# Optimization experiments

Measured on AMD Instinct MI355X. Metric: run time of the kernel, lower is better.

The kernel has to match this reference:

```python
import jax, jax.numpy as jnp
import numpy as np

ROPE_DIMS = 64  # rope_rotary_dims == head_dim, so RoPE covers full head


def fixed_pos_embedding(max_len, rotary_dims):
    inv_freq = 1.0 / (10000 ** (jnp.arange(0, rotary_dims, 2, dtype=jnp.float32) / rotary_dims))
    sinusoid = jnp.einsum('i,j->ij', jnp.arange(max_len, dtype=jnp.float32), inv_freq)
    return jnp.sin(sinusoid), jnp.cos(sinusoid)


def rotate_every_two(x):
    x1 = x[..., ::2]
    x2 = x[..., 1::2]
    return jnp.stack((-x2, x1), axis=-1).reshape(x.shape)


def apply_rotary_pos_emb(x, sin, cos):
    # x: [B, L, H, D]; sin/cos: [L, D//2]
    L = x.shape[1]
    sin = jnp.repeat(sin[:L], 2, axis=-1)[None, :, None, :]  # interleaved repeat == .repeat(2, axis=3)
    cos = jnp.repeat(cos[:L], 2, axis=-1)[None, :, None, :]
    return x * cos + rotate_every_two(x) * sin


def setup_inputs() -> dict:
    key = jax.random.key(0)
    ks = jax.random.split(key, 8)
    B, Lq, Lkv, F, H, D = 2, 2048, 2048, 1024, 16, 64
    s = 0.02
    return {
        'inputs_q': jax.random.normal(ks[0], (B, Lq, F), dtype=jnp.float32),
        'inputs_kv': jax.random.normal(ks[1], (B, Lkv, F), dtype=jnp.float32),
        'mask': jax.random.randint(ks[2], (B, 1, Lq, Lkv), 0, 2) > 0,
        'Wq': jax.random.normal(ks[3], (F, H, D), dtype=jnp.float32) * s,
        'bq': jnp.zeros((H, D), dtype=jnp.float32),
        'Wk': jax.random.normal(ks[4], (F, D), dtype=jnp.float32) * s,
        'bk': jnp.zeros((D,), dtype=jnp.float32),
        'Wv': jax.random.normal(ks[5], (F, D), dtype=jnp.float32) * s,
        'bv': jnp.zeros((D,), dtype=jnp.float32),
        'Wo': jax.random.normal(ks[6], (H, D, F), dtype=jnp.float32) * s,
        'bo': jnp.zeros((F,), dtype=jnp.float32),
    }


def reference(inputs_q, inputs_kv, mask, Wq, bq, Wk, bk, Wv, bv, Wo, bo):
    D = Wq.shape[-1]
    Lq, Lkv = inputs_q.shape[1], inputs_kv.shape[1]
    # QKV projections (multi-query: single shared K/V head)
    q = jnp.einsum('blf,fhd->blhd', inputs_q, Wq) + bq   # [B,Lq,H,D]
    k = jnp.einsum('blf,fd->bld', inputs_kv, Wk) + bk    # [B,Lkv,D]
    v = jnp.einsum('blf,fd->bld', inputs_kv, Wv) + bv    # [B,Lkv,D]
    # RoPE on q and (head-expanded) k
    sin, cos = fixed_pos_embedding(max(Lq, Lkv), ROPE_DIMS)
    q = apply_rotary_pos_emb(q, sin, cos)
    k = apply_rotary_pos_emb(k[:, :, None, :], sin, cos)[:, :, 0, :]
    # multi-query attention
    q = q / jnp.sqrt(jnp.float32(D))
    attn = jnp.einsum('bqhd,bkd->bhqk', q, k)            # [B,H,Lq,Lkv]
    big_neg = jnp.finfo(jnp.float32).min
    attn = jnp.where(mask, attn, big_neg)
    attn = jax.nn.softmax(attn, axis=-1)
    out = jnp.einsum('bhqk,bkd->bqhd', attn, v)          # [B,Lq,H,D]
    # output projection
    return jnp.einsum('bqhd,hdf->bqf', out, Wo) + bo     # [B,Lq,F]
```

## Files before the change

### kernel.cpp

```cpp
#include <hip/hip_runtime.h>

typedef unsigned short u16;
typedef unsigned int u32;
typedef unsigned long long u64;
typedef __bf16 bf16x8 __attribute__((ext_vector_type(8)));
typedef u16 u16x8 __attribute__((ext_vector_type(8)));
typedef float f32x4 __attribute__((ext_vector_type(4)));

__device__ __forceinline__ u16 f2bf(float f) {
    return __builtin_bit_cast(u16, (__bf16)f);
}

__device__ __forceinline__ void gl_lds16(const void* g, void* l) {
    __builtin_amdgcn_global_load_lds(
        (const __attribute__((address_space(1))) unsigned int*)g,
        (__attribute__((address_space(3))) unsigned int*)l, 16, 0, 0);
}

#define QSCALE 0.18033688011112042f

__global__ void detect_mask(const unsigned char* __restrict__ m, int* __restrict__ flag,
                            float* __restrict__ lut) {
    int t = threadIdx.x;
    lut[t] = (((t >> 2) >> (t & 3)) & 1) ? -16.0f : -100000.0f;
    if (t == 0) {
        int any0 = 0, any1 = 0;
        for (int g = 0; g < 64; ++g) {
            any0 |= (m[4 * g] != 0);
            any1 |= (m[4 * g + 1] != 0);
        }
        *flag = any1 ? 0 : (any0 ? 1 : 2);
    }
}

__global__ void prep(const float4* __restrict__ inq, const float4* __restrict__ inkv,
                     ushort4* __restrict__ oAq, ushort4* __restrict__ oAkv,
                     const float* __restrict__ Wq, const float* __restrict__ Wk,
                     const float* __restrict__ Wv, const float* __restrict__ Wo,
                     u16* __restrict__ Wcat, u16* __restrict__ Wot,
                     const void* __restrict__ mask, const int* __restrict__ flagp,
                     u64* __restrict__ Mb, float2* __restrict__ rtbl) {
    int bid = blockIdx.x;
    const int tid = threadIdx.x;
    if (bid < 8192) {
        int i = bid * 256 + tid;
        const float4* src; ushort4* dst; int j;
        if (i < 1048576) { src = inq;  dst = oAq;  j = i; }
        else             { src = inkv; dst = oAkv; j = i - 1048576; }
        float4 f = src[j];
        ushort4 o;
        o.x = f2bf(f.x); o.y = f2bf(f.y); o.z = f2bf(f.z); o.w = f2bf(f.w);
        dst[j] = o;
        return;
    }
    bid -= 8192;
    if (bid < 2176) {
        const float* src; u16* dst; int C, bx, by;
        if (bid < 1024)      { src = Wq; dst = Wcat;           C = 1024; bx = bid & 31;          by = bid >> 5; }
        else if (bid < 2048) { src = Wo; dst = Wot;            C = 1024; bx = (bid - 1024) & 31; by = (bid - 1024) >> 5; }
        else if (bid < 2112) { src = Wk; dst = Wcat + 1048576; C = 64;   bx = (bid - 2048) & 1;  by = (bid - 2048) >> 1; }
        else                 { src = Wv; dst = Wcat + 1114112; C = 64;   bx = (bid - 2112) & 1;  by = (bid - 2112) >> 1; }
        __shared__ float t[32][33];
        int tx = tid & 31, ty = tid >> 5;
        bx *= 32; by *= 32;
#pragma unroll
        for (int i = 0; i < 4; ++i)
            t[ty + i * 8][tx] = src[(size_t)(by + ty + i * 8) * C + bx + tx];
        __syncthreads();
#pragma unroll
        for (int i = 0; i < 4; ++i)
            dst[(size_t)(bx + ty + i * 8) * 1024 + by + tx] = f2bf(t[tx][ty + i * 8]);
        return;
    }
    bid -= 2176;
    if (bid < 256) {
        int i = bid * 256 + tid;
        int pos = i >> 5, j = i & 31;
        float inv = powf(10000.0f, -(float)(2 * j) * (1.0f / 64.0f));
        float s, c;
        sincosf((float)pos * inv, &s, &c);
        rtbl[i] = make_float2(c, s);
        return;
    }
    bid -= 256;
    {
        int flag = *flagp;
        int lane = tid & 63;
        for (int wid = bid * 4 + (tid >> 6); wid < 131072; wid += 8192) {
            size_t idx = (size_t)wid * 64 + lane;
            bool v;
            if (flag == 0)      v = ((const unsigned char*)mask)[idx] != 0;
            else if (flag == 1) v = ((const int*)mask)[idx] != 0;
            else                v = ((const float*)mask)[idx] != 0.f;
            u64 bm = __ballot(v);
            if (lane == 0) Mb[wid] = bm;
        }
    }
}

template <int MODE>
__launch_bounds__(256)
__global__ void gemm_bt(const u16* __restrict__ A0, const u16* __restrict__ A1,
                        const u16* __restrict__ Bt,
                        const float* __restrict__ b1, const float* __restrict__ b2,
                        const float* __restrict__ b3,
                        const float2* __restrict__ rtbl,
                        u16* __restrict__ oQ, u16* __restrict__ oK, u16* __restrict__ oV,
                        float* __restrict__ oF, int Ntiles) {
    __shared__ __align__(16) u16 lA[2][64 * 64];
    __shared__ __align__(16) u16 lB[2][128 * 64];
    const int tid = threadIdx.x, w = tid >> 6, lane = tid & 63;
    const int tm = blockIdx.x / Ntiles, tn = blockIdx.x % Ntiles;
    const int wm = w >> 1, wn = w & 1;
    const int lq = lane & 15, g = lane >> 4, g4 = g << 2;
    const u32 swz = (lane & 7) << 4;
    const u32 bcolg = (16 * g) ^ swz;
    const u16* A = (MODE == 0 && tn == 8) ? A1 : A0;

    const int rA0 = tid >> 3, ch = tid & 7;
    const int rB0 = rA0;
    const u32 offc = ((u32)(ch << 4)) ^ ((u32)((rA0 & 7) << 4));
    const u16* pA0 = A + (size_t)(tm * 64 + rA0) * 1024 + ch * 8;
    const u16* pA1 = pA0 + 32 * 1024;
    const u16* pB0 = Bt + (size_t)(tn * 128 + rB0) * 1024 + ch * 8;
    const u16* pB1 = pB0 + 32 * 1024;
    const u16* pB2 = pB0 + 64 * 1024;
    const u16* pB3 = pB0 + 96 * 1024;
    const u32 offA0 = rA0 * 128 + offc, offA1 = offA0 + 32 * 128;
    const u32 offB0 = offA0, offB1 = offB0 + 32 * 128, offB2 = offB0 + 64 * 128,
              offB3 = offB0 + 96 * 128;

    u16x8 ra0, ra1, rb0, rb1, rb2, rb3;
    f32x4 acc[2][4] = {};

    ra0 = *(const u16x8*)(pA0); ra1 = *(const u16x8*)(pA1);
    rb0 = *(const u16x8*)(pB0); rb1 = *(const u16x8*)(pB1);
    rb2 = *(const u16x8*)(pB2); rb3 = *(const u16x8*)(pB3);
    *(u16x8*)((char*)lA + offA0) = ra0; *(u16x8*)((char*)lA + offA1) = ra1;
    *(u16x8*)((char*)lB + offB0) = rb0; *(u16x8*)((char*)lB + offB1) = rb1;
    *(u16x8*)((char*)lB + offB2) = rb2; *(u16x8*)((char*)lB + offB3) = rb3;
    __syncthreads();

#pragma unroll
    for (int t = 0; t < 16; ++t) {
        if (t < 15) {
            ra0 = *(const u16x8*)(pA0 + (t + 1) * 64); ra1 = *(const u16x8*)(pA1 + (t + 1) * 64);
            rb0 = *(const u16x8*)(pB0 + (t + 1) * 64); rb1 = *(const u16x8*)(pB1 + (t + 1) * 64);
            rb2 = *(const u16x8*)(pB2 + (t + 1) * 64); rb3 = *(const u16x8*)(pB3 + (t + 1) * 64);
        }
        const char* bA = (const char*)lA + (t & 1) * 8192;
        const char* bB = (const char*)lB + (t & 1) * 16384;
#pragma unroll
        for (int kc = 0; kc < 2; ++kc) {
            const u32 col = bcolg ^ (64 * kc);
            bf16x8 af0 = *(const bf16x8*)(bA + (wm * 32 + lq) * 128 + col);
            bf16x8 af1 = *(const bf16x8*)(bA + (wm * 32 + 16 + lq) * 128 + col);
            bf16x8 bg0 = *(const bf16x8*)(bB + (wn * 64 + lq) * 128 + col);
            bf16x8 bg1 = *(const bf16x8*)(bB + (wn * 64 + 16 + lq) * 128 + col);
            bf16x8 bg2 = *(const bf16x8*)(bB + (wn * 64 + 32 + lq) * 128 + col);
            bf16x8 bg3 = *(const bf16x8*)(bB + (wn * 64 + 48 + lq) * 128 + col);
            acc[0][0] = __builtin_amdgcn_mfma_f32_16x16x32_bf16(af0, bg0, acc[0][0], 0, 0, 0);
            acc[0][1] = __builtin_amdgcn_mfma_f32_16x16x32_bf16(af0, bg1, acc[0][1], 0, 0, 0);
            acc[0][2] = __builtin_amdgcn_mfma_f32_16x16x32_bf16(af0, bg2, acc[0][2], 0, 0, 0);
            acc[0][3] = __builtin_amdgcn_mfma_f32_16x16x32_bf16(af0, bg3, acc[0][3], 0, 0, 0);
            acc[1][0] = __builtin_amdgcn_mfma_f32_16x16x32_bf16(af1, bg0, acc[1][0], 0, 0, 0);
            acc[1][1] = __builtin_amdgcn_mfma_f32_16x16x32_bf16(af1, bg1, acc[1][1], 0, 0, 0);
            acc[1][2] = __builtin_amdgcn_mfma_f32_16x16x32_bf16(af1, bg2, acc[1][2], 0, 0, 0);
            acc[1][3] = __builtin_amdgcn_mfma_f32_16x16x32_bf16(af1, bg3, acc[1][3], 0, 0, 0);
        }
        if (t < 15) {
            char* nA = (char*)lA + ((t + 1) & 1) * 8192;
            char* nB = (char*)lB + ((t + 1) & 1) * 16384;
            *(u16x8*)(nA + offA0) = ra0; *(u16x8*)(nA + offA1) = ra1;
            *(u16x8*)(nB + offB0) = rb0; *(u16x8*)(nB + offB1) = rb1;
            *(u16x8*)(nB + offB2) = rb2; *(u16x8*)(nB + offB3) = rb3;
        }
        __syncthreads();
    }

#pragma unroll
    for (int mi = 0; mi < 2; ++mi) {
#pragma unroll
        for (int ni = 0; ni < 4; ++ni) {
#pragma unroll
            for (int r = 0; r < 4; ++r) {
                int grow = tm * 64 + wm * 32 + mi * 16 + g4 + r;
                float v = acc[mi][ni][r];
                if constexpr (MODE == 0) {
                    int pos = grow & 2047;
                    if (tn < 8) {
                        int gcol = tn * 128 + wn * 64 + ni * 16 + lq;
                        v += b1[gcol];
                        float2 cs = rtbl[pos * 32 + ((gcol & 63) >> 1)];
                        float prt = __shfl_xor(v, 1);
                        v = (gcol & 1) ? (v * cs.x + prt * cs.y) : (v * cs.x - prt * cs.y);
                        v *= QSCALE;
                        oQ[(size_t)grow * 1024 + gcol] = f2bf(v);
                    } else {
                        int lc = wn * 64 + ni * 16 + lq;
                        if (lc < 64) {
                            v += b2[lc];
                            float2 cs = rtbl[pos * 32 + (lc >> 1)];
                            float prt = __shfl_xor(v, 1);
                            v = (lc & 1) ? (v * cs.x + prt * cs.y) : (v * cs.x - prt * cs.y);
                            oK[(size_t)grow * 64 + lc] = f2bf(v);
                        } else {
                            int d = lc - 64;
                            v += b3[d];
                            int b = grow >> 11, ll = grow & 2047;
                            oV[((size_t)(b * 64 + d)) * 2048 + ll] = f2bf(v);
                        }
                    }
                } else {
                    int gcol = tn * 128 + wn * 64 + ni * 16 + lq;
                    oF[(size_t)grow * 1024 + gcol] = v + b1[gcol];
                }
            }
        }
    }
}

__launch_bounds__(256, 4)
__global__ void flash(const u16* __restrict__ Qb, const u16* __restrict__ Kb,
                      const u16* __restrict__ Vt, const u64* __restrict__ Mb,
                      const f32x4* __restrict__ lut, u16* __restrict__ Ob) {
    __shared__ __align__(16) u16 lK[2][64 * 64];
    __shared__ __align__(16) u16 lV[2][64 * 64];
    __shared__ __align__(16) u16 lP[4 * 16 * 64];
    const int tid = threadIdx.x, w = tid >> 6, lane = tid & 63;
    const int qt = blockIdx.x & 31, h = (blockIdx.x >> 5) & 15, b = blockIdx.x >> 9;
    const int qb = qt * 64 + w * 16;
    const int lq = lane & 15, g = lane >> 4, g4 = g << 2;
    const u32 swz = (lq & 7) << 4;
    const u32 rowoff = lq * 128;
    const u32 bcol = ((u32)(16 * g)) ^ swz;
    const u32 bw = ((u32)(8 * g)) ^ swz;
    char* lPw = (char*)lP + w * 2048;
    const int sh = 4 * g;

    bf16x8 qf0, qf1;
    {
        const u16* qp = Qb + (size_t)(b * 2048 + qb + lq) * 1024 + h * 64 + g * 8;
        qf0 = *(const bf16x8*)(qp);
        qf1 = *(const bf16x8*)(qp + 32);
    }

    const u64* Mrow = Mb + (size_t)(b * 2048 + qb + lq) * 32;

    const int rs = tid >> 3, ch = tid & 7;
    const u32 scb = (((u32)(ch << 4)) ^ ((u32)((rs & 7) << 4))) >> 1;
    const u16* pK0 = Kb + (size_t)(b * 2048 + rs) * 64 + scb;
    const u16* pK1 = pK0 + 32 * 64;
    const u16* pV0 = Vt + (size_t)(b * 64 + rs) * 2048 + scb;
    const u16* pV1 = pV0 + 32 * 2048;
    char* dK = (char*)lK + tid * 16;
    char* dV = (char*)lV + tid * 16;

#define STAGE(BUF)                                                   \
    {                                                                \
        gl_lds16(pK0, dK + (BUF) * 8192);                            \
        gl_lds16(pK1, dK + (BUF) * 8192 + 4096);                     \
        gl_lds16(pV0, dV + (BUF) * 8192);                            \
        gl_lds16(pV1, dV + (BUF) * 8192 + 4096);                     \
        pK0 += 4096; pK1 += 4096; pV0 += 64; pV1 += 64;              \
    }

    f32x4 o0 = {}, o1 = {}, o2 = {}, o3 = {};
    float lsum = 0.f;

    f32x4 iA0, iA1, iA2, iA3, iB0, iB1, iB2, iB3;
    u64 mwA, mwB;
    {
        u64 ms = Mrow[0] >> sh;
        u32 lo = (u32)ms, hi = (u32)(ms >> 32);
        iA0 = lut[lo & 15]; iA1 = lut[(lo >> 16) & 15];
        iA2 = lut[hi & 15]; iA3 = lut[(hi >> 16) & 15];
    }
    mwA = Mrow[1];
    STAGE(0);
    __syncthreads();

#define EXPPK(NF, S)                                                                    \
    {                                                                                   \
        float p0 = exp2f(S[0]), p1 = exp2f(S[1]), p2 = exp2f(S[2]), p3 = exp2f(S[3]);   \
        lsum += (p0 + p1) + (p2 + p3);                                                  \
        uint2 pk_;                                                                      \
        pk_.x = (u32)f2bf(p0) | ((u32)f2bf(p1) << 16);                                  \
        pk_.y = (u32)f2bf(p2) | ((u32)f2bf(p3) << 16);                                  \
        *(uint2*)(lPw + rowoff + (bw ^ (32 * NF))) = pk_;                               \
    }

#define COMPUTE(BUF, I0, I1, I2, I3, N0, N1, N2, N3, MWC, MWN, KC)                      \
    {                                                                                   \
        MWN = Mrow[(KC) + 2];                                                           \
        {                                                                               \
            u64 ms = MWC >> sh;                                                         \
            u32 lo = (u32)ms, hi = (u32)(ms >> 32);                                     \
            N0 = lut[lo & 15]; N1 = lut[(lo >> 16) & 15];                               \
            N2 = lut[hi & 15]; N3 = lut[(hi >> 16) & 15];                               \
        }                                                                               \
        f32x4 s0 = I0, s1 = I1, s2 = I2, s3 = I3;                                       \
        {                                                                               \
            const char* kb_ = (const char*)lK + (BUF) * 8192 + rowoff;                  \
            bf16x8 k00 = *(const bf16x8*)(kb_ + bcol);                                  \
            bf16x8 k01 = *(const bf16x8*)(kb_ + (bcol ^ 64));                           \
            bf16x8 k10 = *(const bf16x8*)(kb_ + 2048 + bcol);                           \
            bf16x8 k11 = *(const bf16x8*)(kb_ + 2048 + (bcol ^ 64));                    \
            bf16x8 k20 = *(const bf16x8*)(kb_ + 4096 + bcol);                           \
            bf16x8 k21 = *(const bf16x8*)(kb_ + 4096 + (bcol ^ 64));                    \
            bf16x8 k30 = *(const bf16x8*)(kb_ + 6144 + bcol);                           \
            bf16x8 k31 = *(const bf16x8*)(kb_ + 6144 + (bcol ^ 64));                    \
            s0 = __builtin_amdgcn_mfma_f32_16x16x32_bf16(k00, qf0, s0, 0, 0, 0);        \
            s0 = __builtin_amdgcn_mfma_f32_16x16x32_bf16(k01, qf1, s0, 0, 0, 0);        \
            s1 = __builtin_amdgcn_mfma_f32_16x16x32_bf16(k10, qf0, s1, 0, 0, 0);        \
            s1 = __builtin_amdgcn_mfma_f32_16x16x32_bf16(k11, qf1, s1, 0, 0, 0);        \
            s2 = __builtin_amdgcn_mfma_f32_16x16x32_bf16(k20, qf0, s2, 0, 0, 0);        \
            s2 = __builtin_amdgcn_mfma_f32_16x16x32_bf16(k21, qf1, s2, 0, 0, 0);        \
            s3 = __builtin_amdgcn_mfma_f32_16x16x32_bf16(k30, qf0, s3, 0, 0, 0);        \
            s3 = __builtin_amdgcn_mfma_f32_16x16x32_bf16(k31, qf1, s3, 0, 0, 0);        \
        }                                                                               \
        EXPPK(0, s0) EXPPK(1, s1) EXPPK(2, s2) EXPPK(3, s3)                             \
        {                                                                               \
            bf16x8 pf0 = *(const bf16x8*)(lPw + rowoff + bcol);                         \
            bf16x8 pf1 = *(const bf16x8*)(lPw + rowoff + (bcol ^ 64));                  \
            const char* vb_ = (const char*)lV + (BUF) * 8192 + rowoff;                  \
            bf16x8 v00 = *(const bf16x8*)(vb_ + bcol);                                  \
            bf16x8 v01 = *(const bf16x8*)(vb_ + (bcol ^ 64));                           \
            bf16x8 v10 = *(const bf16x8*)(vb_ + 2048 + bcol);                           \
            bf16x8 v11 = *(const bf16x8*)(vb_ + 2048 + (bcol ^ 64));                    \
            bf16x8 v20 = *(const bf16x8*)(vb_ + 4096 + bcol);                           \
            bf16x8 v21 = *(const bf16x8*)(vb_ + 4096 + (bcol ^ 64));                    \
            bf16x8 v30 = *(const bf16x8*)(vb_ + 6144 + bcol);                           \
            bf16x8 v31 = *(const bf16x8*)(vb_ + 6144 + (bcol ^ 64));                    \
            o0 = __builtin_amdgcn_mfma_f32_16x16x32_bf16(pf0, v00, o0, 0, 0, 0);        \
            o0 = __builtin_amdgcn_mfma_f32_16x16x32_bf16(pf1, v01, o0, 0, 0, 0);        \
            o1 = __builtin_amdgcn_mfma_f32_16x16x32_bf16(pf0, v10, o1, 0, 0, 0);        \
            o1 = __builtin_amdgcn_mfma_f32_16x16x32_bf16(pf1, v11, o1, 0, 0, 0);        \
            o2 = __builtin_amdgcn_mfma_f32_16x16x32_bf16(pf0, v20, o2, 0, 0, 0);        \
            o2 = __builtin_amdgcn_mfma_f32_16x16x32_bf16(pf1, v21, o2, 0, 0, 0);        \
            o3 = __builtin_amdgcn_mfma_f32_16x16x32_bf16(pf0, v30, o3, 0, 0, 0);        \
            o3 = __builtin_amdgcn_mfma_f32_16x16x32_bf16(pf1, v31, o3, 0, 0, 0);        \
        }                                                                               \
    }

    for (int kc = 0; kc < 32; kc += 2) {
        STAGE(1);
        COMPUTE(0, iA0, iA1, iA2, iA3, iB0, iB1, iB2, iB3, mwA, mwB, kc);
        __syncthreads();
        STAGE(0);
        COMPUTE(1, iB0, iB1, iB2, iB3, iA0, iA1, iA2, iA3, mwB, mwA, kc + 1);
        __syncthreads();
    }
#undef STAGE
#undef COMPUTE
#undef EXPPK

    lsum += __shfl_xor(lsum, 16);
    lsum += __shfl_xor(lsum, 32);
    float rl0 = 1.0f / __shfl(lsum, g4);
    float rl1 = 1.0f / __shfl(lsum, g4 + 1);
    float rl2 = 1.0f / __shfl(lsum, g4 + 2);
    float rl3 = 1.0f / __shfl(lsum, g4 + 3);
    {
        int col = h * 64 + lq;
        size_t base = (size_t)(b * 2048 + qb + g4) * 1024 + col;
        Ob[base]              = f2bf(o0[0] * rl0);
        Ob[base + 1024]       = f2bf(o0[1] * rl1);
        Ob[base + 2048]       = f2bf(o0[2] * rl2);
        Ob[base + 3072]       = f2bf(o0[3] * rl3);
        Ob[base + 16]         = f2bf(o1[0] * rl0);
        Ob[base + 16 + 1024]  = f2bf(o1[1] * rl1);
        Ob[base + 16 + 2048]  = f2bf(o1[2] * rl2);
        Ob[base + 16 + 3072]  = f2bf(o1[3] * rl3);
        Ob[base + 32]         = f2bf(o2[0] * rl0);
        Ob[base + 32 + 1024]  = f2bf(o2[1] * rl1);
        Ob[base + 32 + 2048]  = f2bf(o2[2] * rl2);
        Ob[base + 32 + 3072]  = f2bf(o2[3] * rl3);
        Ob[base + 48]         = f2bf(o3[0] * rl0);
        Ob[base + 48 + 1024]  = f2bf(o3[1] * rl1);
        Ob[base + 48 + 2048]  = f2bf(o3[2] * rl2);
        Ob[base + 48 + 3072]  = f2bf(o3[3] * rl3);
    }
}

extern "C" void kernel_launch(void* const* d_in, const int* in_sizes, int n_in,
                              void* d_out, int out_size, void* d_ws, size_t ws_size,
                              hipStream_t stream) {
    (void)in_sizes; (void)n_in; (void)out_size; (void)ws_size;
    const float* inq  = (const float*)d_in[0];
    const float* inkv = (const float*)d_in[1];
    const void*  mask = d_in[2];
    const float* Wq   = (const float*)d_in[3];
    const float* bq   = (const float*)d_in[4];
    const float* Wk   = (const float*)d_in[5];
    const float* bk   = (const float*)d_in[6];
    const float* Wv   = (const float*)d_in[7];
    const float* bv   = (const float*)d_in[8];
    const float* Wo   = (const float*)d_in[9];
    const float* bo   = (const float*)d_in[10];
    float* out = (float*)d_out;

    char* ws = (char*)d_ws;
    int* flag    = (int*)ws;
    f32x4* lut   = (f32x4*)(ws + 256);
    u16* Aq   = (u16*)(ws + 512);
    u16* Akv  = Aq + 4194304;
    u16* Wcat = Akv + 4194304;
    u16* Wot  = Wcat + 1179648;
    u16* Qb   = Wot + 1048576;
    u16* Kbf  = Qb + 4194304;
    u16* Vtb  = Kbf + 266496;
    u16* Ob   = Vtb + 266496;
    u64* Mb   = (u64*)(Ob + 4194304);
    float2* rtbl = (float2*)(Mb + 131080);

    detect_mask<<<1, 64, 0, stream>>>((const unsigned char*)mask, flag, (float*)lut);
    prep<<<12672, 256, 0, stream>>>((const float4*)inq, (const float4*)inkv,
                                    (ushort4*)Aq, (ushort4*)Akv,
                                    Wq, Wk, Wv, Wo, Wcat, Wot,
                                    mask, flag, Mb, rtbl);
    gemm_bt<0><<<576, 256, 0, stream>>>(Aq, Akv, Wcat, bq, bk, bv, rtbl,
                                        Qb, Kbf, Vtb, nullptr, 9);
    flash<<<1024, 256, 0, stream>>>(Qb, Kbf, Vtb, Mb, lut, Ob);
    gemm_bt<2><<<512, 256, 0, stream>>>(Ob, nullptr, Wot, bo, nullptr, nullptr, rtbl,
                                        nullptr, nullptr, nullptr, out, 8);
}
```

Before: 139.1 us.

## Rewrite flash attention with 32x32 MFMA, register-resident P, swizzled K/V layout

Result: slower. 153.2 us (+10.1%).

```diff
diff --git a/kernel.cpp b/kernel.cpp
--- a/kernel.cpp
+++ b/kernel.cpp
@@ -4,8 +4,11 @@
 typedef unsigned int u32;
 typedef unsigned long long u64;
 typedef __bf16 bf16x8 __attribute__((ext_vector_type(8)));
+typedef __bf16 bf16x4 __attribute__((ext_vector_type(4)));
 typedef u16 u16x8 __attribute__((ext_vector_type(8)));
 typedef float f32x4 __attribute__((ext_vector_type(4)));
+typedef float f32x16 __attribute__((ext_vector_type(16)));
+typedef u32 u32x4 __attribute__((ext_vector_type(4)));
 
 __device__ __forceinline__ u16 f2bf(float f) {
     return __builtin_bit_cast(u16, (__bf16)f);
@@ -118,11 +121,10 @@
     const u16* A = (MODE == 0 && tn == 8) ? A1 : A0;
 
     const int rA0 = tid >> 3, ch = tid & 7;
-    const int rB0 = rA0;
     const u32 offc = ((u32)(ch << 4)) ^ ((u32)((rA0 & 7) << 4));
     const u16* pA0 = A + (size_t)(tm * 64 + rA0) * 1024 + ch * 8;
     const u16* pA1 = pA0 + 32 * 1024;
-    const u16* pB0 = Bt + (size_t)(tn * 128 + rB0) * 1024 + ch * 8;
+    const u16* pB0 = Bt + (size_t)(tn * 128 + rA0) * 1024 + ch * 8;
     const u16* pB1 = pB0 + 32 * 1024;
     const u16* pB2 = pB0 + 64 * 1024;
     const u16* pB3 = pB0 + 96 * 1024;
@@ -203,12 +205,15 @@
                             float2 cs = rtbl[pos * 32 + (lc >> 1)];
                             float prt = __shfl_xor(v, 1);
                             v = (lc & 1) ? (v * cs.x + prt * cs.y) : (v * cs.x - prt * cs.y);
-                            oK[(size_t)grow * 64 + lc] = f2bf(v);
+                            oK[(size_t)grow * 64 + ((((u32)lc >> 2) ^ ((u32)grow & 15)) << 2)
+                               + (lc & 3)] = f2bf(v);
                         } else {
                             int d = lc - 64;
                             v += b3[d];
                             int b = grow >> 11, ll = grow & 2047;
-                            oV[((size_t)(b * 64 + d)) * 2048 + ll] = f2bf(v);
+                            int cc = ll & 63;
+                            oV[((size_t)(b * 64 + d)) * 2048 + (ll & ~63)
+                               + ((((u32)cc >> 2) ^ ((u32)d & 15)) << 2) + (cc & 3)] = f2bf(v);
                         }
                     }
                 } else {
@@ -220,166 +225,163 @@
     }
 }
 
-__launch_bounds__(256, 4)
+#define MFMA32(A, B, C) __builtin_amdgcn_mfma_f32_32x32x16_bf16(A, B, C, 0, 0, 0)
+
+__launch_bounds__(256)
 __global__ void flash(const u16* __restrict__ Qb, const u16* __restrict__ Kb,
                       const u16* __restrict__ Vt, const u64* __restrict__ Mb,
                       const f32x4* __restrict__ lut, u16* __restrict__ Ob) {
     __shared__ __align__(16) u16 lK[2][64 * 64];
     __shared__ __align__(16) u16 lV[2][64 * 64];
-    __shared__ __align__(16) u16 lP[4 * 16 * 64];
     const int tid = threadIdx.x, w = tid >> 6, lane = tid & 63;
-    const int qt = blockIdx.x & 31, h = (blockIdx.x >> 5) & 15, b = blockIdx.x >> 9;
-    const int qb = qt * 64 + w * 16;
-    const int lq = lane & 15, g = lane >> 4, g4 = g << 2;
-    const u32 swz = (lq & 7) << 4;
-    const u32 rowoff = lq * 128;
-    const u32 bcol = ((u32)(16 * g)) ^ swz;
-    const u32 bw = ((u32)(8 * g)) ^ swz;
-    char* lPw = (char*)lP + w * 2048;
-    const int sh = 4 * g;
-
-    bf16x8 qf0, qf1;
+    const int qt = blockIdx.x & 15, hh = (blockIdx.x >> 4) & 15, b = blockIdx.x >> 8;
+    const int qb = qt * 128 + w * 32;
+    const int l31 = lane & 31, h = lane >> 5, l15 = lane & 15;
+
+    bf16x8 qf0, qf1, qf2, qf3;
     {
-        const u16* qp = Qb + (size_t)(b * 2048 + qb + lq) * 1024 + h * 64 + g * 8;
+        const u16* qp = Qb + (size_t)(b * 2048 + qb + l31) * 1024 + hh * 64 + h * 8;
         qf0 = *(const bf16x8*)(qp);
-        qf1 = *(const bf16x8*)(qp + 32);
-    }
-
-    const u64* Mrow = Mb + (size_t)(b * 2048 + qb + lq) * 32;
-
-    const int rs = tid >> 3, ch = tid & 7;
-    const u32 scb = (((u32)(ch << 4)) ^ ((u32)((rs & 7) << 4))) >> 1;
-    const u16* pK0 = Kb + (size_t)(b * 2048 + rs) * 64 + scb;
-    const u16* pK1 = pK0 + 32 * 64;
-    const u16* pV0 = Vt + (size_t)(b * 64 + rs) * 2048 + scb;
-    const u16* pV1 = pV0 + 32 * 2048;
-    char* dK = (char*)lK + tid * 16;
-    char* dV = (char*)lV + tid * 16;
-
-#define STAGE(BUF)                                                   \
-    {                                                                \
-        gl_lds16(pK0, dK + (BUF) * 8192);                            \
-        gl_lds16(pK1, dK + (BUF) * 8192 + 4096);                     \
-        gl_lds16(pV0, dV + (BUF) * 8192);                            \
-        gl_lds16(pV1, dV + (BUF) * 8192 + 4096);                     \
-        pK0 += 4096; pK1 += 4096; pV0 += 64; pV1 += 64;              \
-    }
-
-    f32x4 o0 = {}, o1 = {}, o2 = {}, o3 = {};
+        qf1 = *(const bf16x8*)(qp + 16);
+        qf2 = *(const bf16x8*)(qp + 32);
+        qf3 = *(const bf16x8*)(qp + 48);
+    }
+
+    const u64* Mrow = Mb + (size_t)(b * 2048 + qb + l31) * 32;
+
+    u32 dof0 = ((u32)(2 * h) ^ l15) << 3,      dof1 = ((u32)(2 * h + 1) ^ l15) << 3;
+    u32 dof2 = ((u32)(4 + 2 * h) ^ l15) << 3,  dof3 = ((u32)(5 + 2 * h) ^ l15) << 3;
+    u32 dof4 = ((u32)(8 + 2 * h) ^ l15) << 3,  dof5 = ((u32)(9 + 2 * h) ^ l15) << 3;
+    u32 dof6 = ((u32)(12 + 2 * h) ^ l15) << 3, dof7 = ((u32)(13 + 2 * h) ^ l15) << 3;
+    const char* kvbase = (const char*)lK + l31 * 128;
+
+    const u16* pK = Kb + (size_t)b * 131072 + tid * 8;
+    const u16* pV = Vt + (size_t)(b * 64 + (tid >> 3)) * 2048 + (tid & 7) * 8;
+    const u16* pV2 = pV + 32 * 2048;
+
+#define STAGE(BUF)                                                       \
+    {                                                                    \
+        gl_lds16(pK,        (char*)lK + (BUF) * 8192 + tid * 16);        \
+        gl_lds16(pK + 2048, (char*)lK + (BUF) * 8192 + 4096 + tid * 16); \
+        gl_lds16(pV,        (char*)lV + (BUF) * 8192 + tid * 16);        \
+        gl_lds16(pV2,       (char*)lV + (BUF) * 8192 + 4096 + tid * 16); \
+        pK += 4096; pV += 64; pV2 += 64;                                 \
+    }
+
+    f32x16 o0 = {}, o1 = {};
+    f32x16 cin0, cin1;
     float lsum = 0.f;
-
-    f32x4 iA0, iA1, iA2, iA3, iB0, iB1, iB2, iB3;
-    u64 mwA, mwB;
-    {
-        u64 ms = Mrow[0] >> sh;
-        u32 lo = (u32)ms, hi = (u32)(ms >> 32);
-        iA0 = lut[lo & 15]; iA1 = lut[(lo >> 16) & 15];
-        iA2 = lut[hi & 15]; iA3 = lut[(hi >> 16) & 15];
-    }
-    mwA = Mrow[1];
+    u64 mw;
+
+#define BUILD_CIN(MW)                                                        \
+    {                                                                        \
+        u64 ms_ = (MW) >> (4 * h);                                           \
+        _Pragma("unroll") for (int rg = 0; rg < 4; ++rg) {                   \
+            f32x4 e0_ = lut[(u32)((ms_ >> (8 * rg)) & 15)];                  \
+            f32x4 e1_ = lut[(u32)((ms_ >> (32 + 8 * rg)) & 15)];             \
+            cin0[4 * rg] = e0_[0]; cin0[4 * rg + 1] = e0_[1];                \
+            cin0[4 * rg + 2] = e0_[2]; cin0[4 * rg + 3] = e0_[3];            \
+            cin1[4 * rg] = e1_[0]; cin1[4 * rg + 1] = e1_[1];                \
+            cin1[4 * rg + 2] = e1_[2]; cin1[4 * rg + 3] = e1_[3];            \
+        }                                                                    \
+    }
+
+#define FRAG(DST, IMM, OFA, OFB)                                             \
+    {                                                                        \
+        bf16x4 lo_ = *(const bf16x4*)(kvbase + (IMM) + (OFA));               \
+        bf16x4 hi_ = *(const bf16x4*)(kvbase + (IMM) + (OFB));               \
+        DST = __builtin_shufflevector(lo_, hi_, 0, 1, 2, 3, 4, 5, 6, 7);     \
+    }
+
+#define PK2(A, B) ((u32)f2bf(A) | ((u32)f2bf(B) << 16))
+#define MKPA(PA, E0, E1, E2, E3, E4, E5, E6, E7)                             \
+    {                                                                        \
+        u32 x0_ = PK2(E0, E1), x1_ = PK2(E2, E3);                            \
+        u32 y0_ = PK2(E4, E5), y1_ = PK2(E6, E7);                            \
+        asm("v_permlane32_swap_b32 %0, %1" : "+v"(x0_), "+v"(y0_));          \
+        asm("v_permlane32_swap_b32 %0, %1" : "+v"(x1_), "+v"(y1_));          \
+        u32x4 t_ = {x0_, x1_, y0_, y1_};                                     \
+        PA = __builtin_bit_cast(bf16x8, t_);                                 \
+    }
+
+#define CHUNK(BUF, KC)                                                                   \
+    {                                                                                    \
+        if ((KC) < 31) STAGE((BUF) ^ 1);                                                 \
+        f32x16 st0 = cin0, st1 = cin1;                                                   \
+        {                                                                                \
+            bf16x8 kf;                                                                   \
+            FRAG(kf, (BUF) * 8192,        dof0, dof1); st0 = MFMA32(kf, qf0, st0);       \
+            FRAG(kf, (BUF) * 8192,        dof2, dof3); st0 = MFMA32(kf, qf1, st0);       \
+            FRAG(kf, (BUF) * 8192,        dof4, dof5); st0 = MFMA32(kf, qf2, st0);       \
+            FRAG(kf, (BUF) * 8192,        dof6, dof7); st0 = MFMA32(kf, qf3, st0);       \
+            FRAG(kf, (BUF) * 8192 + 4096, dof0, dof1); st1 = MFMA32(kf, qf0, st1);       \
+            FRAG(kf, (BUF) * 8192 + 4096, dof2, dof3); st1 = MFMA32(kf, qf1, st1);       \
+            FRAG(kf, (BUF) * 8192 + 4096, dof4, dof5); st1 = MFMA32(kf, qf2, st1);       \
+            FRAG(kf, (BUF) * 8192 + 4096, dof6, dof7); st1 = MFMA32(kf, qf3, st1);       \
+        }                                                                                \
+        float e0 = exp2f(st0[0]), e1 = exp2f(st0[1]), e2 = exp2f(st0[2]),                \
+              e3 = exp2f(st0[3]), e4 = exp2f(st0[4]), e5 = exp2f(st0[5]),                \
+              e6 = exp2f(st0[6]), e7 = exp2f(st0[7]), e8 = exp2f(st0[8]),                \
+              e9 = exp2f(st0[9]), e10 = exp2f(st0[10]), e11 = exp2f(st0[11]),            \
+              e12 = exp2f(st0[12]), e13 = exp2f(st0[13]), e14 = exp2f(st0[14]),          \
+              e15 = exp2f(st0[15]);                                                      \
+        float f0 = exp2f(st1[0]), f1 = exp2f(st1[1]), f2 = exp2f(st1[2]),                \
+              f3 = exp2f(st1[3]), f4 = exp2f(st1[4]), f5 = exp2f(st1[5]),                \
+              f6 = exp2f(st1[6]), f7 = exp2f(st1[7]), f8 = exp2f(st1[8]),                \
+              f9 = exp2f(st1[9]), f10 = exp2f(st1[10]), f11 = exp2f(st1[11]),            \
+              f12 = exp2f(st1[12]), f13 = exp2f(st1[13]), f14 = exp2f(st1[14]),          \
+              f15 = exp2f(st1[15]);                                                      \
+        lsum += (((e0 + e1) + (e2 + e3)) + ((e4 + e5) + (e6 + e7))) +                    \
+                (((e8 + e9) + (e10 + e11)) + ((e12 + e13) + (e14 + e15))) +              \
+                (((f0 + f1) + (f2 + f3)) + ((f4 + f5) + (f6 + f7))) +                    \
+                (((f8 + f9) + (f10 + f11)) + ((f12 + f13) + (f14 + f15)));               \
+        bf16x8 pa0, pa1, pa2, pa3;                                                       \
+        MKPA(pa0, e0, e1, e2, e3, e4, e5, e6, e7);                                       \
+        MKPA(pa1, e8, e9, e10, e11, e12, e13, e14, e15);                                 \
+        MKPA(pa2, f0, f1, f2, f3, f4, f5, f6, f7);                                       \
+        MKPA(pa3, f8, f9, f10, f11, f12, f13, f14, f15);                                 \
+        BUILD_CIN(mw);                                                                   \
+        mw = Mrow[(KC) + 2];                                                             \
+        {                                                                                \
+            bf16x8 vv;                                                                   \
+            FRAG(vv, 16384 + (BUF) * 8192,        dof0, dof1); o0 = MFMA32(pa0, vv, o0); \
+            FRAG(vv, 16384 + (BUF) * 8192,        dof2, dof3); o0 = MFMA32(pa1, vv, o0); \
+            FRAG(vv, 16384 + (BUF) * 8192,        dof4, dof5); o0 = MFMA32(pa2, vv, o0); \
+            FRAG(vv, 16384 + (BUF) * 8192,        dof6, dof7); o0 = MFMA32(pa3, vv, o0); \
+            FRAG(vv, 16384 + (BUF) * 8192 + 4096, dof0, dof1); o1 = MFMA32(pa0, vv, o1); \
+            FRAG(vv, 16384 + (BUF) * 8192 + 4096, dof2, dof3); o1 = MFMA32(pa1, vv, o1); \
+            FRAG(vv, 16384 + (BUF) * 8192 + 4096, dof4, dof5); o1 = MFMA32(pa2, vv, o1); \
+            FRAG(vv, 16384 + (BUF) * 8192 + 4096, dof6, dof7); o1 = MFMA32(pa3, vv, o1); \
+        }                                                                                \
+        __syncthreads();                                                                 \
+    }
+
     STAGE(0);
+    mw = Mrow[0];
+    BUILD_CIN(mw);
+    mw = Mrow[1];
     __syncthreads();
 
-#define EXPPK(NF, S)                                                                    \
-    {                                                                                   \
-        float p0 = exp2f(S[0]), p1 = exp2f(S[1]), p2 = exp2f(S[2]), p3 = exp2f(S[3]);   \
-        lsum += (p0 + p1) + (p2 + p3);                                                  \
-        uint2 pk_;                                                                      \
-        pk_.x = (u32)f2bf(p0) | ((u32)f2bf(p1) << 16);                                  \
-        pk_.y = (u32)f2bf(p2) | ((u32)f2bf(p3) << 16);                                  \
-        *(uint2*)(lPw + rowoff + (bw ^ (32 * NF))) = pk_;                               \
-    }
-
-#define COMPUTE(BUF, I0, I1, I2, I3, N0, N1, N2, N3, MWC, MWN, KC)                      \
-    {                                                                                   \
-        MWN = Mrow[(KC) + 2];                                                           \
-        {                                                                               \
-            u64 ms = MWC >> sh;                                                         \
-            u32 lo = (u32)ms, hi = (u32)(ms >> 32);                                     \
-            N0 = lut[lo & 15]; N1 = lut[(lo >> 16) & 15];                               \
-            N2 = lut[hi & 15]; N3 = lut[(hi >> 16) & 15];                               \
-        }                                                                               \
-        f32x4 s0 = I0, s1 = I1, s2 = I2, s3 = I3;                                       \
-        {                                                                               \
-            const char* kb_ = (const char*)lK + (BUF) * 8192 + rowoff;                  \
-            bf16x8 k00 = *(const bf16x8*)(kb_ + bcol);                                  \
-            bf16x8 k01 = *(const bf16x8*)(kb_ + (bcol ^ 64));                           \
-            bf16x8 k10 = *(const bf16x8*)(kb_ + 2048 + bcol);                           \
-            bf16x8 k11 = *(const bf16x8*)(kb_ + 2048 + (bcol ^ 64));                    \
-            bf16x8 k20 = *(const bf16x8*)(kb_ + 4096 + bcol);                           \
-            bf16x8 k21 = *(const bf16x8*)(kb_ + 4096 + (bcol ^ 64));                    \
-            bf16x8 k30 = *(const bf16x8*)(kb_ + 6144 + bcol);                           \
-            bf16x8 k31 = *(const bf16x8*)(kb_ + 6144 + (bcol ^ 64));                    \
-            s0 = __builtin_amdgcn_mfma_f32_16x16x32_bf16(k00, qf0, s0, 0, 0, 0);        \
-            s0 = __builtin_amdgcn_mfma_f32_16x16x32_bf16(k01, qf1, s0, 0, 0, 0);        \
-            s1 = __builtin_amdgcn_mfma_f32_16x16x32_bf16(k10, qf0, s1, 0, 0, 0);        \
-            s1 = __builtin_amdgcn_mfma_f32_16x16x32_bf16(k11, qf1, s1, 0, 0, 0);        \
-            s2 = __builtin_amdgcn_mfma_f32_16x16x32_bf16(k20, qf0, s2, 0, 0, 0);        \
-            s2 = __builtin_amdgcn_mfma_f32_16x16x32_bf16(k21, qf1, s2, 0, 0, 0);        \
-            s3 = __builtin_amdgcn_mfma_f32_16x16x32_bf16(k30, qf0, s3, 0, 0, 0);        \
-            s3 = __builtin_amdgcn_mfma_f32_16x16x32_bf16(k31, qf1, s3, 0, 0, 0);        \
-        }                                                                               \
-        EXPPK(0, s0) EXPPK(1, s1) EXPPK(2, s2) EXPPK(3, s3)                             \
-        {                                                                               \
-            bf16x8 pf0 = *(const bf16x8*)(lPw + rowoff + bcol);                         \
-            bf16x8 pf1 = *(const bf16x8*)(lPw + rowoff + (bcol ^ 64));                  \
-            const char* vb_ = (const char*)lV + (BUF) * 8192 + rowoff;                  \
-            bf16x8 v00 = *(const bf16x8*)(vb_ + bcol);                                  \
-            bf16x8 v01 = *(const bf16x8*)(vb_ + (bcol ^ 64));                           \
-            bf16x8 v10 = *(const bf16x8*)(vb_ + 2048 + bcol);                           \
-            bf16x8 v11 = *(const bf16x8*)(vb_ + 2048 + (bcol ^ 64));                    \
-            bf16x8 v20 = *(const bf16x8*)(vb_ + 4096 + bcol);                           \
-            bf16x8 v21 = *(const bf16x8*)(vb_ + 4096 + (bcol ^ 64));                    \
-            bf16x8 v30 = *(const bf16x8*)(vb_ + 6144 + bcol);                           \
-            bf16x8 v31 = *(const bf16x8*)(vb_ + 6144 + (bcol ^ 64));                    \
-            o0 = __builtin_amdgcn_mfma_f32_16x16x32_bf16(pf0, v00, o0, 0, 0, 0);        \
-            o0 = __builtin_amdgcn_mfma_f32_16x16x32_bf16(pf1, v01, o0, 0, 0, 0);        \
-            o1 = __builtin_amdgcn_mfma_f32_16x16x32_bf16(pf0, v10, o1, 0, 0, 0);        \
-            o1 = __builtin_amdgcn_mfma_f32_16x16x32_bf16(pf1, v11, o1, 0, 0, 0);        \
-            o2 = __builtin_amdgcn_mfma_f32_16x16x32_bf16(pf0, v20, o2, 0, 0, 0);        \
-            o2 = __builtin_amdgcn_mfma_f32_16x16x32_bf16(pf1, v21, o2, 0, 0, 0);        \
-            o3 = __builtin_amdgcn_mfma_f32_16x16x32_bf16(pf0, v30, o3, 0, 0, 0);        \
-            o3 = __builtin_amdgcn_mfma_f32_16x16x32_bf16(pf1, v31, o3, 0, 0, 0);        \
-        }                                                                               \
-    }
-
-    for (int kc = 0; kc < 32; kc += 2) {
-        STAGE(1);
-        COMPUTE(0, iA0, iA1, iA2, iA3, iB0, iB1, iB2, iB3, mwA, mwB, kc);
-        __syncthreads();
-        STAGE(0);
-        COMPUTE(1, iB0, iB1, iB2, iB3, iA0, iA1, iA2, iA3, mwB, mwA, kc + 1);
-        __syncthreads();
+    for (int t2 = 0; t2 < 16; ++t2) {
+        CHUNK(0, 2 * t2);
+        CHUNK(1, 2 * t2 + 1);
     }
 #undef STAGE
-#undef COMPUTE
-#undef EXPPK
-
-    lsum += __shfl_xor(lsum, 16);
+#undef CHUNK
+#undef BUILD_CIN
+#undef FRAG
+#undef MKPA
+#undef PK2
+
     lsum += __shfl_xor(lsum, 32);
-    float rl0 = 1.0f / __shfl(lsum, g4);
-    float rl1 = 1.0f / __shfl(lsum, g4 + 1);
-    float rl2 = 1.0f / __shfl(lsum, g4 + 2);
-    float rl3 = 1.0f / __shfl(lsum, g4 + 3);
-    {
-        int col = h * 64 + lq;
-        size_t base = (size_t)(b * 2048 + qb + g4) * 1024 + col;
-        Ob[base]              = f2bf(o0[0] * rl0);
-        Ob[base + 1024]       = f2bf(o0[1] * rl1);
-        Ob[base + 2048]       = f2bf(o0[2] * rl2);
-        Ob[base + 3072]       = f2bf(o0[3] * rl3);
-        Ob[base + 16]         = f2bf(o1[0] * rl0);
-        Ob[base + 16 + 1024]  = f2bf(o1[1] * rl1);
-        Ob[base + 16 + 2048]  = f2bf(o1[2] * rl2);
-        Ob[base + 16 + 3072]  = f2bf(o1[3] * rl3);
-        Ob[base + 32]         = f2bf(o2[0] * rl0);
-        Ob[base + 32 + 1024]  = f2bf(o2[1] * rl1);
-        Ob[base + 32 + 2048]  = f2bf(o2[2] * rl2);
-        Ob[base + 32 + 3072]  = f2bf(o2[3] * rl3);
-        Ob[base + 48]         = f2bf(o3[0] * rl0);
-        Ob[base + 48 + 1024]  = f2bf(o3[1] * rl1);
-        Ob[base + 48 + 2048]  = f2bf(o3[2] * rl2);
-        Ob[base + 48 + 3072]  = f2bf(o3[3] * rl3);
+    float rl = 1.0f / lsum;
+    const size_t obase = (size_t)(b * 2048 + qb) * 1024 + hh * 64 + l31;
+#pragma unroll
+    for (int r = 0; r < 16; ++r) {
+        int qloc = (r & 3) + 8 * (r >> 2) + 4 * h;
+        float rq = __shfl(rl, qloc);
+        Ob[obase + (size_t)qloc * 1024]      = f2bf(o0[r] * rq);
+        Ob[obase + (size_t)qloc * 1024 + 32] = f2bf(o1[r] * rq);
     }
 }
 
@@ -421,7 +423,7 @@
                                     mask, flag, Mb, rtbl);
     gemm_bt<0><<<576, 256, 0, stream>>>(Aq, Akv, Wcat, bq, bk, bv, rtbl,
                                         Qb, Kbf, Vtb, nullptr, 9);
-    flash<<<1024, 256, 0, stream>>>(Qb, Kbf, Vtb, Mb, lut, Ob);
+    flash<<<512, 256, 0, stream>>>(Qb, Kbf, Vtb, Mb, lut, Ob);
     gemm_bt<2><<<512, 256, 0, stream>>>(Ob, nullptr, Wot, bo, nullptr, nullptr, rtbl,
                                         nullptr, nullptr, nullptr, out, 8);
 }
```
